# Kernel tuning notes

Hardware: AMD Instinct MI355X
Metric: run time of the kernel (lower is better)

## Reference

```python
import jax, jax.numpy as jnp
import numpy as np

TEMPERATURE = 0.07
EPS = 1e-12  # F.normalize default eps

def _l2norm(x):
    n = jnp.linalg.norm(x, axis=1, keepdims=True)
    return x / jnp.maximum(n, EPS)

def setup_inputs() -> dict:
    key = jax.random.key(0)
    k1, k2 = jax.random.split(key)
    N, D = 16384, 256
    return {
        "feat_local": jax.random.normal(k1, (N, D), dtype=jnp.float32),
        "feat_global": jax.random.normal(k2, (N, D), dtype=jnp.float32),
    }

def reference(feat_local, feat_global):
    fl = _l2norm(feat_local)
    fg = _l2norm(feat_global)
    # [N, N] similarity matrix scaled by temperature
    sim = jnp.einsum('nd,md->nm', fl, fg) / TEMPERATURE
    pos_sim = jnp.diagonal(sim)
    loss = -pos_sim + jax.scipy.special.logsumexp(sim, axis=1)
    return loss.mean()
```

## Files before the change

### kernel.cpp

```cpp
#include <hip/hip_runtime.h>
#include <hip/hip_bf16.h>

#define NROWS 16384
#define DIM   256
#define SEGS  8
#define BN    128
#define NT    ((NROWS / SEGS) / BN)
#define INVT  14.285714285714286f
#define C1f   20.60992915555662f
#define LN2f  0.6931471805599453f

typedef __attribute__((ext_vector_type(8)))  int   int8v;
typedef __attribute__((ext_vector_type(16))) float f32x16;

#define SCALE1 0x7F7F7F7F

__global__ __launch_bounds__(256) void norm_diag_kernel(
    const float* __restrict__ fl, const float* __restrict__ fg,
    unsigned char* __restrict__ A, unsigned char* __restrict__ B,
    float* __restrict__ diag, float* __restrict__ out)
{
    int tid  = threadIdx.x;
    int wave = tid >> 6, lane = tid & 63;
    int row  = blockIdx.x * 4 + wave;
    if (blockIdx.x == 0 && tid == 0) out[0] = 0.0f;

    float4 xl = ((const float4*)(fl + (size_t)row * DIM))[lane];
    float4 xg = ((const float4*)(fg + (size_t)row * DIM))[lane];
    float ssl = xl.x*xl.x + xl.y*xl.y + xl.z*xl.z + xl.w*xl.w;
    float ssg = xg.x*xg.x + xg.y*xg.y + xg.z*xg.z + xg.w*xg.w;
    for (int m = 1; m < 64; m <<= 1) {
        ssl += __shfl_xor(ssl, m, 64);
        ssg += __shfl_xor(ssg, m, 64);
    }
    float il = 1.0f / fmaxf(sqrtf(ssl), 1e-12f);
    float ig = 1.0f / fmaxf(sqrtf(ssg), 1e-12f);
    float nl0 = xl.x*il, nl1 = xl.y*il, nl2 = xl.z*il, nl3 = xl.w*il;
    float ng0 = xg.x*ig, ng1 = xg.y*ig, ng2 = xg.z*ig, ng3 = xg.w*ig;

    int pa = __builtin_amdgcn_cvt_pk_fp8_f32(nl0 * C1f, nl1 * C1f, 0, false);
    pa     = __builtin_amdgcn_cvt_pk_fp8_f32(nl2 * C1f, nl3 * C1f, pa, true);
    int pb = __builtin_amdgcn_cvt_pk_fp8_f32(ng0, ng1, 0, false);
    pb     = __builtin_amdgcn_cvt_pk_fp8_f32(ng2, ng3, pb, true);
    ((int*)(A + (size_t)row * DIM))[lane] = pa;

    {
        int kcb = lane >> 2;
        int b4  = lane & 3;
        unsigned chunk = (unsigned)((row >> 7) * 2048 + ((row >> 6) & 1) * 1024
                                    + kcb * 64 + (row & 63));
        ((int*)B)[chunk * 4 + b4] = pb;
    }

    float d = nl0*ng0 + nl1*ng1 + nl2*ng2 + nl3*ng3;
    for (int m = 1; m < 64; m <<= 1) d += __shfl_xor(d, m, 64);
    if (lane == 0) diag[row] = d;
}

__global__ __launch_bounds__(256, 2) void sim_lse_kernel(
    const unsigned char* __restrict__ A, const unsigned char* __restrict__ B,
    float* __restrict__ lpart)
{
    __shared__ __align__(16) unsigned char bt[2 * BN * DIM];

    int tid  = threadIdx.x;
    int lane = tid & 63;
    int l31  = lane & 31, half = lane >> 5;
    int wave = tid >> 6;
    int seg  = blockIdx.x;
    int rowBase = blockIdx.y * 256 + wave * 64;

    unsigned vb = (unsigned)(l31 * 16 + half * 2048);

    int8v af[2][4];
#pragma unroll
    for (int s = 0; s < 2; ++s) {
        const unsigned char* ap = A + (size_t)(rowBase + s*32 + l31) * DIM + half * 32;
#pragma unroll
        for (int kk = 0; kk < 4; ++kk) {
            int4 lo = *(const int4*)(ap + kk * 64);
            int4 hi = *(const int4*)(ap + kk * 64 + 16);
            int8v v;
            v[0]=lo.x; v[1]=lo.y; v[2]=lo.z; v[3]=lo.w;
            v[4]=hi.x; v[5]=hi.y; v[6]=hi.z; v[7]=hi.w;
            af[s][kk] = v;
        }
    }

    f32x16 lv[2];
    f32x16 Z;
    f32x16 accA[2], accB[2];
#pragma unroll
    for (int r = 0; r < 16; ++r) {
        lv[0][r] = -1.0f; lv[1][r] = -1.0f;
        Z[r] = 0.0f;
        accB[0][r] = 0.0f; accB[1][r] = 0.0f;
    }

    int T0 = seg * NT;

    auto stage = [&](int T, unsigned bufo) {
        const unsigned char* g = B + (size_t)T * (BN * DIM) + (wave * 512 + lane) * 16;
        unsigned lo = bufo + (unsigned)(wave * 512) * 16;
#pragma unroll
        for (int j = 0; j < 8; ++j) {
            __builtin_amdgcn_global_load_lds(
                (const __attribute__((address_space(1))) unsigned int*)(g + j * 1024),
                (__attribute__((address_space(3))) unsigned int*)&bt[lo + j * 1024],
                16, 0, 0);
        }
    };

    auto chain = [&](f32x16 (&ac)[2], unsigned ab, unsigned offc) {
        int8v bf[4];
#pragma unroll
        for (int kk = 0; kk < 4; ++kk) {
            int4 lo = *(const int4*)&bt[ab + offc + (unsigned)kk * 4096u];
            int4 hi = *(const int4*)&bt[ab + offc + (unsigned)kk * 4096u + 1024u];
            int8v v;
            v[0]=lo.x; v[1]=lo.y; v[2]=lo.z; v[3]=lo.w;
            v[4]=hi.x; v[5]=hi.y; v[6]=hi.z; v[7]=hi.w;
            bf[kk] = v;
        }
        ac[0] = __builtin_amdgcn_mfma_scale_f32_32x32x64_f8f6f4(
            af[0][0], bf[0], Z, 0, 0, 0, SCALE1, 0, SCALE1);
        ac[1] = __builtin_amdgcn_mfma_scale_f32_32x32x64_f8f6f4(
            af[1][0], bf[0], Z, 0, 0, 0, SCALE1, 0, SCALE1);
#pragma unroll
        for (int kk = 1; kk < 4; ++kk) {
            ac[0] = __builtin_amdgcn_mfma_scale_f32_32x32x64_f8f6f4(
                af[0][kk], bf[kk], ac[0], 0, 0, 0, SCALE1, 0, SCALE1);
            ac[1] = __builtin_amdgcn_mfma_scale_f32_32x32x64_f8f6f4(
                af[1][kk], bf[kk], ac[1], 0, 0, 0, SCALE1, 0, SCALE1);
        }
    };

    auto epi = [&](f32x16 (&ac)[2]) {
#pragma unroll
        for (int s = 0; s < 2; ++s) {
            f32x16 e;
#pragma unroll
            for (int r = 0; r < 16; ++r)
                e[r] = __builtin_amdgcn_exp2f(ac[s][r]);
            lv[s] += e;
        }
    };

    stage(T0, 0);

    for (int t = 0; t < NT; ++t) {
        unsigned bufo = (t & 1) ? (unsigned)(BN * DIM) : 0u;
        __syncthreads();

        if (t + 1 < NT)
            stage(T0 + t + 1, (t & 1) ? 0u : (unsigned)(BN * DIM));

        unsigned ab = vb + bufo;
        chain(accA, ab, 0u);      epi(accB);
        chain(accB, ab, 512u);    epi(accA);
        chain(accA, ab, 16384u);  epi(accB);
        chain(accB, ab, 16896u);  epi(accA);

#pragma unroll
        for (int gidx = 0; gidx < 32; ++gidx) {
            __builtin_amdgcn_sched_group_barrier(0x100, 2, 0);
            __builtin_amdgcn_sched_group_barrier(0x008, 1, 0);
            __builtin_amdgcn_sched_group_barrier(0x002, 8, 0);
        }
    }
    epi(accB);

#pragma unroll
    for (int s = 0; s < 2; ++s)
#pragma unroll
        for (int r = 0; r < 16; ++r) {
            float v = lv[s][r];
            v += __shfl_xor(v, 1, 64);
            v += __shfl_xor(v, 2, 64);
            v += __shfl_xor(v, 4, 64);
            v += __shfl_xor(v, 8, 64);
            v += __shfl_xor(v, 16, 64);
            lv[s][r] = v;
        }
    if (l31 == 0) {
#pragma unroll
        for (int s = 0; s < 2; ++s)
#pragma unroll
            for (int r = 0; r < 16; ++r) {
                int row = rowBase + s*32 + (r & 3) + 8*(r >> 2) + 4*half;
                lpart[(size_t)seg * NROWS + row] = lv[s][r];
            }
    }
}

__global__ __launch_bounds__(256) void reduce_kernel(
    const float* __restrict__ lpart, const float* __restrict__ diag,
    float* __restrict__ out)
{
    __shared__ float sm[4];
    int gtid = blockIdx.x * 256 + threadIdx.x;
    float s = 0.0f;
    for (int row = gtid; row < NROWS; row += 32 * 256) {
        float t = 0.0f;
#pragma unroll
        for (int g = 0; g < SEGS; ++g) t += lpart[(size_t)g * NROWS + row];
        s += LN2f * log2f(t) - INVT * diag[row];
    }
    for (int m = 1; m < 64; m <<= 1) s += __shfl_xor(s, m, 64);
    int wave = threadIdx.x >> 6, lane = threadIdx.x & 63;
    if (lane == 0) sm[wave] = s;
    __syncthreads();
    if (threadIdx.x == 0) {
        float tot = sm[0] + sm[1] + sm[2] + sm[3];
        atomicAdd(out, tot * (1.0f / NROWS));
    }
}

extern "C" void kernel_launch(void* const* d_in, const int* in_sizes, int n_in,
                              void* d_out, int out_size, void* d_ws, size_t ws_size,
                              hipStream_t stream) {
    const float* fl = (const float*)d_in[0];
    const float* fg = (const float*)d_in[1];
    float* out = (float*)d_out;

    char* ws = (char*)d_ws;
    unsigned char* A = (unsigned char*)ws;
    unsigned char* B = A + (size_t)NROWS * DIM;
    float* diag  = (float*)(ws + 2 * (size_t)NROWS * DIM);
    float* lpart = diag + NROWS;

    norm_diag_kernel<<<NROWS / 4, 256, 0, stream>>>(fl, fg, A, B, diag, out);
    sim_lse_kernel<<<dim3(SEGS, NROWS / 256), 256, 0, stream>>>(A, B, lpart);
    reduce_kernel<<<32, 256, 0, stream>>>(lpart, diag, out);
}
```

Before: 141.0 us.

## Split sim kernel into MFMA producer and exp consumer warps via LDS

The similarity kernel becomes warp-specialized, with 8 waves per block. Four waves run the FP8 MFMA chains and write their accumulators into double-buffered LDS slots. The other four waves issue the B-tile async loads, read the accumulators back, and apply exp2 to accumulate row sums. The intent is to run the transcendental epilogue in parallel with the matrix cores instead of interleaving both in the same waves. The cost is 128KB of shared memory per block, four barriers per tile, and extra LDS write/read traffic for every accumulator, which likely leaves only one block resident per CU.

New measurement: 167.3 us. 1.19x slower.

```diff
diff --git a/kernel.cpp b/kernel.cpp
--- a/kernel.cpp
+++ b/kernel.cpp
@@ -14,6 +14,8 @@
 typedef __attribute__((ext_vector_type(16))) float f32x16;
 
 #define SCALE1 0x7F7F7F7F
+#define ACC0   65536u
+#define ACC1   98304u
 
 __global__ __launch_bounds__(256) void norm_diag_kernel(
     const float* __restrict__ fl, const float* __restrict__ fg,
@@ -57,51 +59,51 @@
     if (lane == 0) diag[row] = d;
 }
 
-__global__ __launch_bounds__(256, 2) void sim_lse_kernel(
+__global__ __launch_bounds__(512, 2) void sim_lse_kernel(
     const unsigned char* __restrict__ A, const unsigned char* __restrict__ B,
     float* __restrict__ lpart)
 {
-    __shared__ __align__(16) unsigned char bt[2 * BN * DIM];
+    __shared__ __align__(16) unsigned char bt[4 * BN * DIM];
 
     int tid  = threadIdx.x;
     int lane = tid & 63;
     int l31  = lane & 31, half = lane >> 5;
     int wave = tid >> 6;
+    bool isExp = (wave >= 4);
+    int rw   = wave & 3;
     int seg  = blockIdx.x;
-    int rowBase = blockIdx.y * 256 + wave * 64;
+    int rowBase = blockIdx.y * 256 + rw * 64;
 
     unsigned vb = (unsigned)(l31 * 16 + half * 2048);
+    unsigned accOff = (unsigned)(rw * 8192 + lane * 16);
 
     int8v af[2][4];
-#pragma unroll
-    for (int s = 0; s < 2; ++s) {
-        const unsigned char* ap = A + (size_t)(rowBase + s*32 + l31) * DIM + half * 32;
-#pragma unroll
-        for (int kk = 0; kk < 4; ++kk) {
-            int4 lo = *(const int4*)(ap + kk * 64);
-            int4 hi = *(const int4*)(ap + kk * 64 + 16);
-            int8v v;
-            v[0]=lo.x; v[1]=lo.y; v[2]=lo.z; v[3]=lo.w;
-            v[4]=hi.x; v[5]=hi.y; v[6]=hi.z; v[7]=hi.w;
-            af[s][kk] = v;
+    if (!isExp) {
+#pragma unroll
+        for (int s = 0; s < 2; ++s) {
+            const unsigned char* ap = A + (size_t)(rowBase + s*32 + l31) * DIM + half * 32;
+#pragma unroll
+            for (int kk = 0; kk < 4; ++kk) {
+                int4 lo = *(const int4*)(ap + kk * 64);
+                int4 hi = *(const int4*)(ap + kk * 64 + 16);
+                int8v v;
+                v[0]=lo.x; v[1]=lo.y; v[2]=lo.z; v[3]=lo.w;
+                v[4]=hi.x; v[5]=hi.y; v[6]=hi.z; v[7]=hi.w;
+                af[s][kk] = v;
+            }
         }
     }
 
     f32x16 lv[2];
     f32x16 Z;
-    f32x16 accA[2], accB[2];
-#pragma unroll
-    for (int r = 0; r < 16; ++r) {
-        lv[0][r] = -1.0f; lv[1][r] = -1.0f;
-        Z[r] = 0.0f;
-        accB[0][r] = 0.0f; accB[1][r] = 0.0f;
-    }
+#pragma unroll
+    for (int r = 0; r < 16; ++r) { lv[0][r] = 0.0f; lv[1][r] = 0.0f; Z[r] = 0.0f; }
 
     int T0 = seg * NT;
 
     auto stage = [&](int T, unsigned bufo) {
-        const unsigned char* g = B + (size_t)T * (BN * DIM) + (wave * 512 + lane) * 16;
-        unsigned lo = bufo + (unsigned)(wave * 512) * 16;
+        const unsigned char* g = B + (size_t)T * (BN * DIM) + (rw * 512 + lane) * 16;
+        unsigned lo = bufo + (unsigned)(rw * 512) * 16;
 #pragma unroll
         for (int j = 0; j < 8; ++j) {
             __builtin_amdgcn_global_load_lds(
@@ -111,7 +113,7 @@
         }
     };
 
-    auto chain = [&](f32x16 (&ac)[2], unsigned ab, unsigned offc) {
+    auto produce = [&](unsigned ab, unsigned offc, unsigned accb) {
         int8v bf[4];
 #pragma unroll
         for (int kk = 0; kk < 4; ++kk) {
@@ -122,74 +124,86 @@
             v[4]=hi.x; v[5]=hi.y; v[6]=hi.z; v[7]=hi.w;
             bf[kk] = v;
         }
-        ac[0] = __builtin_amdgcn_mfma_scale_f32_32x32x64_f8f6f4(
+        f32x16 a0, a1;
+        a0 = __builtin_amdgcn_mfma_scale_f32_32x32x64_f8f6f4(
             af[0][0], bf[0], Z, 0, 0, 0, SCALE1, 0, SCALE1);
-        ac[1] = __builtin_amdgcn_mfma_scale_f32_32x32x64_f8f6f4(
+        a1 = __builtin_amdgcn_mfma_scale_f32_32x32x64_f8f6f4(
             af[1][0], bf[0], Z, 0, 0, 0, SCALE1, 0, SCALE1);
 #pragma unroll
         for (int kk = 1; kk < 4; ++kk) {
-            ac[0] = __builtin_amdgcn_mfma_scale_f32_32x32x64_f8f6f4(
-                af[0][kk], bf[kk], ac[0], 0, 0, 0, SCALE1, 0, SCALE1);
-            ac[1] = __builtin_amdgcn_mfma_scale_f32_32x32x64_f8f6f4(
-                af[1][kk], bf[kk], ac[1], 0, 0, 0, SCALE1, 0, SCALE1);
+            a0 = __builtin_amdgcn_mfma_scale_f32_32x32x64_f8f6f4(
+                af[0][kk], bf[kk], a0, 0, 0, 0, SCALE1, 0, SCALE1);
+            a1 = __builtin_amdgcn_mfma_scale_f32_32x32x64_f8f6f4(
+                af[1][kk], bf[kk], a1, 0, 0, 0, SCALE1, 0, SCALE1);
+        }
+        unsigned wb = accb + accOff;
+#pragma unroll
+        for (int k = 0; k < 4; ++k) {
+            *(float4*)&bt[wb + (unsigned)k * 1024u] =
+                make_float4(a0[k*4+0], a0[k*4+1], a0[k*4+2], a0[k*4+3]);
+            *(float4*)&bt[wb + 4096u + (unsigned)k * 1024u] =
+                make_float4(a1[k*4+0], a1[k*4+1], a1[k*4+2], a1[k*4+3]);
         }
     };
 
-    auto epi = [&](f32x16 (&ac)[2]) {
-#pragma unroll
-        for (int s = 0; s < 2; ++s) {
-            f32x16 e;
-#pragma unroll
-            for (int r = 0; r < 16; ++r)
-                e[r] = __builtin_amdgcn_exp2f(ac[s][r]);
-            lv[s] += e;
-        }
+    auto consume = [&](unsigned accb) {
+        unsigned rb = accb + accOff;
+#pragma unroll
+        for (int s = 0; s < 2; ++s)
+#pragma unroll
+            for (int k = 0; k < 4; ++k) {
+                float4 v = *(const float4*)&bt[rb + (unsigned)s * 4096u + (unsigned)k * 1024u];
+                lv[s][k*4+0] += __builtin_amdgcn_exp2f(v.x);
+                lv[s][k*4+1] += __builtin_amdgcn_exp2f(v.y);
+                lv[s][k*4+2] += __builtin_amdgcn_exp2f(v.z);
+                lv[s][k*4+3] += __builtin_amdgcn_exp2f(v.w);
+            }
     };
 
-    stage(T0, 0);
+    if (isExp) stage(T0, 0);
 
     for (int t = 0; t < NT; ++t) {
-        unsigned bufo = (t & 1) ? (unsigned)(BN * DIM) : 0u;
-        __syncthreads();
-
-        if (t + 1 < NT)
-            stage(T0 + t + 1, (t & 1) ? 0u : (unsigned)(BN * DIM));
-
+        unsigned bufo = (t & 1) ? 32768u : 0u;
         unsigned ab = vb + bufo;
-        chain(accA, ab, 0u);      epi(accB);
-        chain(accB, ab, 512u);    epi(accA);
-        chain(accA, ab, 16384u);  epi(accB);
-        chain(accB, ab, 16896u);  epi(accA);
-
-#pragma unroll
-        for (int gidx = 0; gidx < 32; ++gidx) {
-            __builtin_amdgcn_sched_group_barrier(0x100, 2, 0);
-            __builtin_amdgcn_sched_group_barrier(0x008, 1, 0);
-            __builtin_amdgcn_sched_group_barrier(0x002, 8, 0);
-        }
-    }
-    epi(accB);
-
-#pragma unroll
-    for (int s = 0; s < 2; ++s)
-#pragma unroll
-        for (int r = 0; r < 16; ++r) {
-            float v = lv[s][r];
-            v += __shfl_xor(v, 1, 64);
-            v += __shfl_xor(v, 2, 64);
-            v += __shfl_xor(v, 4, 64);
-            v += __shfl_xor(v, 8, 64);
-            v += __shfl_xor(v, 16, 64);
-            lv[s][r] = v;
-        }
-    if (l31 == 0) {
+#pragma unroll
+        for (int u = 0; u < 4; ++u) {
+            __syncthreads();
+            if (isExp) {
+                if (u == 0 && t + 1 < NT)
+                    stage(T0 + t + 1, (t & 1) ? 0u : 32768u);
+                if (t > 0 || u > 0)
+                    consume((u & 1) ? ACC0 : ACC1);
+            } else {
+                unsigned offc = (unsigned)((u & 1) * 512 + (u >> 1) * 16384);
+                produce(ab, offc, (u & 1) ? ACC1 : ACC0);
+            }
+        }
+    }
+    __syncthreads();
+    if (isExp) {
+        consume(ACC1);
+
 #pragma unroll
         for (int s = 0; s < 2; ++s)
 #pragma unroll
             for (int r = 0; r < 16; ++r) {
-                int row = rowBase + s*32 + (r & 3) + 8*(r >> 2) + 4*half;
-                lpart[(size_t)seg * NROWS + row] = lv[s][r];
-            }
+                float v = lv[s][r];
+                v += __shfl_xor(v, 1, 64);
+                v += __shfl_xor(v, 2, 64);
+                v += __shfl_xor(v, 4, 64);
+                v += __shfl_xor(v, 8, 64);
+                v += __shfl_xor(v, 16, 64);
+                lv[s][r] = v;
+            }
+        if (l31 == 0) {
+#pragma unroll
+            for (int s = 0; s < 2; ++s)
+#pragma unroll
+                for (int r = 0; r < 16; ++r) {
+                    int row = rowBase + s*32 + (r & 3) + 8*(r >> 2) + 4*half;
+                    lpart[(size_t)seg * NROWS + row] = lv[s][r];
+                }
+        }
     }
 }
 
@@ -230,6 +244,6 @@
     float* lpart = diag + NROWS;
 
     norm_diag_kernel<<<NROWS / 4, 256, 0, stream>>>(fl, fg, A, B, diag, out);
-    sim_lse_kernel<<<dim3(SEGS, NROWS / 256), 256, 0, stream>>>(A, B, lpart);
+    sim_lse_kernel<<<dim3(SEGS, NROWS / 256), 512, 0, stream>>>(A, B, lpart);
     reduce_kernel<<<32, 256, 0, stream>>>(lpart, diag, out);
 }
```
